# Kernel optimization log

Measured on AMD Instinct MI355X. Metric: run time of the kernel, lower is better.

The kernel has to match this reference:

```python
import jax, jax.numpy as jnp
import numpy as np

INPUT_LEN = 24
HIDDEN = 64
BATCH = 8192


def _lstm_layer(seq, Wih, Whh, bih, bhh):
    """Single torch-style LSTM layer. seq: [T, B, in] -> hs: [T, B, H].
    Gate order matches torch: i, f, g, o."""
    B = seq.shape[1]
    H = Whh.shape[1]
    b = bih + bhh
    h0 = jnp.zeros((B, H), seq.dtype)
    c0 = jnp.zeros((B, H), seq.dtype)

    def step(carry, x_t):
        h, c = carry
        gates = x_t @ Wih.T + h @ Whh.T + b  # [B, 4H]
        i, f, g, o = jnp.split(gates, 4, axis=-1)
        c = jax.nn.sigmoid(f) * c + jax.nn.sigmoid(i) * jnp.tanh(g)
        h = jax.nn.sigmoid(o) * jnp.tanh(c)
        return (h, c), h

    _, hs = jax.lax.scan(step, (h0, c0), seq)
    return hs


def setup_inputs() -> dict:
    key = jax.random.key(0)
    ks = jax.random.split(key, 16)
    H = HIDDEN
    s = 1.0 / np.sqrt(H)  # torch LSTM/Linear init scale
    u = lambda k, shape, sc: jax.random.uniform(k, shape, jnp.float32, -sc, sc)
    return {
        "x": jax.random.normal(ks[0], (BATCH, INPUT_LEN), jnp.float32),
        # LSTM layer 0 (input size 1)
        "Wih0": u(ks[1], (4 * H, 1), s),
        "Whh0": u(ks[2], (4 * H, H), s),
        "bih0": u(ks[3], (4 * H,), s),
        "bhh0": u(ks[4], (4 * H,), s),
        # LSTM layer 1 (input size H)
        "Wih1": u(ks[5], (4 * H, H), s),
        "Whh1": u(ks[6], (4 * H, H), s),
        "bih1": u(ks[7], (4 * H,), s),
        "bhh1": u(ks[8], (4 * H,), s),
        # predictor MLP: Linear(H,32) -> ReLU -> Linear(32,1)
        "W1": u(ks[9], (32, H), s),
        "b1": u(ks[10], (32,), s),
        "W2": u(ks[11], (1, 32), 1.0 / np.sqrt(32)),
        "b2": u(ks[12], (1,), 1.0 / np.sqrt(32)),
        "damping": jnp.asarray(0.1, jnp.float32),
        "steps": 20,
    }


def reference(x, Wih0, Whh0, bih0, bhh0, Wih1, Whh1, bih1, bhh1,
              W1, b1, W2, b2, damping, steps):
    cur = x[..., None]  # [B, T, 1]
    alpha = jax.nn.sigmoid(damping)
    preds = []
    prev = None
    for _ in range(steps):
        seq = jnp.transpose(cur, (1, 0, 2))  # [T, B, 1]
        h1 = _lstm_layer(seq, Wih0, Whh0, bih0, bhh0)   # [T, B, H]
        h2 = _lstm_layer(h1, Wih1, Whh1, bih1, bhh1)     # [T, B, H]
        last = h2[-1]                                     # [B, H]
        pred = jax.nn.relu(last @ W1.T + b1) @ W2.T + b2  # [B, 1]
        if prev is not None:
            # torch: pred*(1-alpha) + predictions[-1].detach()*alpha*0.5
            pred = pred * (1.0 - alpha) + jax.lax.stop_gradient(prev) * alpha * 0.5
        preds.append(pred)
        prev = pred
        cur = jnp.concatenate([cur[:, 1:, :], pred[:, None, :]], axis=1)
    return jnp.concatenate(preds, axis=1)  # [B, steps]
```

## Files before the change

kernel.cpp:

```cpp
#include <hip/hip_runtime.h>


typedef _Float16 f16x8 __attribute__((ext_vector_type(8)));
typedef float f32x4 __attribute__((ext_vector_type(4)));

#define NBLK 512
#define NTHR 256
#define SRB  160

__device__ __forceinline__ float sigm(float x) {
  float e = __builtin_amdgcn_exp2f(-1.44269504089f * x);
  return __builtin_amdgcn_rcpf(1.0f + e);
}
__device__ __forceinline__ f32x4 mfma16(uint4 a, uint4 b, f32x4 c) {
  return __builtin_amdgcn_mfma_f32_16x16x32_f16(
      __builtin_bit_cast(f16x8, a), __builtin_bit_cast(f16x8, b), c, 0, 0, 0);
}
__device__ __forceinline__ uint4 pack8s(const float* p, float s) {
  union { uint4 u; _Float16 h[8]; } r;
  #pragma unroll
  for (int i = 0; i < 8; ++i) r.h[i] = (_Float16)(p[i] * s);
  return r.u;
}

__global__ __launch_bounds__(NTHR, 2) void lstm_forecast(
    const float* __restrict__ x,
    const float* __restrict__ Wih0, const float* __restrict__ Whh0,
    const float* __restrict__ bih0, const float* __restrict__ bhh0,
    const float* __restrict__ Wih1, const float* __restrict__ Whh1,
    const float* __restrict__ bih1, const float* __restrict__ bhh1,
    const float* __restrict__ W1,   const float* __restrict__ b1,
    const float* __restrict__ W2,   const float* __restrict__ b2,
    const float* __restrict__ damping, const int* __restrict__ stepsPtr,
    float* __restrict__ out)
{
  __shared__ __align__(16) _Float16 h1s[2][16 * 80];
  __shared__ __align__(16) _Float16 h2s[2][16 * 80];
  __shared__ __align__(16) float    win[24 * 16];
  __shared__ __align__(16) float    pm[2][16];

  const int tid  = threadIdx.x;
  const int wave = tid >> 6;
  const int lane = tid & 63;
  const int cc   = lane & 15;
  const int hi   = lane >> 4;
  const int b0g  = blockIdx.x * 16;

  const float LOG2E = 1.44269504089f;

  uint4 wB0[4][2], wB1[4][2], wB2[4][2];
  float bias0v[4], wih0v[4];
  f32x4 bi1[4];
  #pragma unroll
  for (int gt = 0; gt < 4; ++gt) {
    float sc = (gt == 2) ? 2.0f * LOG2E : LOG2E;
    int row = (wave + 4 * gt) * 16 + cc;
    #pragma unroll
    for (int f = 0; f < 2; ++f) {
      int col = f * 32 + hi * 8;
      wB0[gt][f] = pack8s(Whh0 + row * 64 + col, sc);
      wB1[gt][f] = pack8s(Wih1 + row * 64 + col, sc);
      wB2[gt][f] = pack8s(Whh1 + row * 64 + col, sc);
    }
    bias0v[gt] = (bih0[row] + bhh0[row]) * sc;
    wih0v[gt]  = Wih0[row] * sc;
    float b1c  = (bih1[row] + bhh1[row]) * sc;
    #pragma unroll
    for (int r = 0; r < 4; ++r) bi1[gt][r] = b1c;
  }
  uint4 wM[2];
  {
    int row = (wave & 1) * 16 + cc;
    wM[0] = pack8s(W1 + row * 64 + hi * 8, 1.0f);
    wM[1] = pack8s(W1 + row * 64 + 32 + hi * 8, 1.0f);
  }
  const float w2v  = W2[(wave & 1) * 16 + cc];
  const float b1vv = b1[(wave & 1) * 16 + cc];
  const float alpha  = sigm(damping[0]);
  const int   nsteps = stepsPtr[0];
  const float b2v    = b2[0];

  for (int e = tid; e < 384; e += NTHR) {
    int b = e & 15, t = e >> 4;
    win[t * 16 + b] = x[(b0g + b) * 24 + t];
  }
  __syncthreads();

  float prevp = 0.0f;

  for (int s = 0; s < nsteps; ++s) {
    float c1[4] = {0, 0, 0, 0}, c2s[4] = {0, 0, 0, 0};

    {
      float4 xw = *(const float4*)&win[(s % 24) * 16 + hi * 4];
      float xr[4] = {xw.x, xw.y, xw.z, xw.w};
      #pragma unroll
      for (int r = 0; r < 4; ++r) {
        float a0 = fmaf(xr[r], wih0v[0], bias0v[0]);
        float a1 = fmaf(xr[r], wih0v[1], bias0v[1]);
        float a2 = fmaf(xr[r], wih0v[2], bias0v[2]);
        float a3 = fmaf(xr[r], wih0v[3], bias0v[3]);
        float ig = __builtin_amdgcn_rcpf(1.0f + __builtin_amdgcn_exp2f(-a0));
        float fg = __builtin_amdgcn_rcpf(1.0f + __builtin_amdgcn_exp2f(-a1));
        float gg = __builtin_amdgcn_rcpf(1.0f + __builtin_amdgcn_exp2f(-a2)) * 2.0f - 1.0f;
        float og = __builtin_amdgcn_rcpf(1.0f + __builtin_amdgcn_exp2f(-a3));
        float cv = fmaf(fg, c1[r], ig * gg);
        c1[r] = cv;
        float e2 = __builtin_amdgcn_exp2f(-2.88539008178f * cv);
        float hv = og * (__builtin_amdgcn_rcpf(1.0f + e2) * 2.0f - 1.0f);
        *(_Float16*)((char*)h1s[0] + (hi * 4 + r) * SRB + (wave * 16 + cc) * 2) =
            (_Float16)hv;
      }
    }
    __syncthreads();
    uint4 a1lo = *(uint4*)((char*)h1s[0] + cc * SRB + hi * 16);
    uint4 a1hi = *(uint4*)((char*)h1s[0] + cc * SRB + hi * 16 + 64);
    uint4 a2lo = make_uint4(0, 0, 0, 0), a2hi = make_uint4(0, 0, 0, 0);

    for (int t = 0; t < 23; ++t) {
      int pb = (t + 1) & 1;
      int ph = s + t + 1; if (ph >= 24) ph -= 24;
      float4 xw = *(const float4*)&win[ph * 16 + hi * 4];
      float xr[4] = {xw.x, xw.y, xw.z, xw.w};

      f32x4 acc1[4], acc0[4];
      #pragma unroll
      for (int gt = 0; gt < 4; ++gt) {
        f32x4 tv = mfma16(a1lo, wB1[gt][0], bi1[gt]);
        tv = mfma16(a1hi, wB1[gt][1], tv);
        tv = mfma16(a2lo, wB2[gt][0], tv);
        acc1[gt] = mfma16(a2hi, wB2[gt][1], tv);
      }
      #pragma unroll
      for (int gt = 0; gt < 4; ++gt) {
        f32x4 ai;
        #pragma unroll
        for (int r = 0; r < 4; ++r) ai[r] = fmaf(xr[r], wih0v[gt], bias0v[gt]);
        f32x4 tv = mfma16(a1lo, wB0[gt][0], ai);
        acc0[gt] = mfma16(a1hi, wB0[gt][1], tv);
      }

      #pragma unroll
      for (int r = 0; r < 4; ++r) {
        float ig = __builtin_amdgcn_rcpf(1.0f + __builtin_amdgcn_exp2f(-acc1[0][r]));
        float fg = __builtin_amdgcn_rcpf(1.0f + __builtin_amdgcn_exp2f(-acc1[1][r]));
        float gg = __builtin_amdgcn_rcpf(1.0f + __builtin_amdgcn_exp2f(-acc1[2][r])) * 2.0f - 1.0f;
        float og = __builtin_amdgcn_rcpf(1.0f + __builtin_amdgcn_exp2f(-acc1[3][r]));
        float cv = fmaf(fg, c2s[r], ig * gg);
        c2s[r] = cv;
        float e2 = __builtin_amdgcn_exp2f(-2.88539008178f * cv);
        float hv = og * (__builtin_amdgcn_rcpf(1.0f + e2) * 2.0f - 1.0f);
        *(_Float16*)((char*)h2s[pb] + (hi * 4 + r) * SRB + (wave * 16 + cc) * 2) =
            (_Float16)hv;
      }
      #pragma unroll
      for (int r = 0; r < 4; ++r) {
        float ig = __builtin_amdgcn_rcpf(1.0f + __builtin_amdgcn_exp2f(-acc0[0][r]));
        float fg = __builtin_amdgcn_rcpf(1.0f + __builtin_amdgcn_exp2f(-acc0[1][r]));
        float gg = __builtin_amdgcn_rcpf(1.0f + __builtin_amdgcn_exp2f(-acc0[2][r])) * 2.0f - 1.0f;
        float og = __builtin_amdgcn_rcpf(1.0f + __builtin_amdgcn_exp2f(-acc0[3][r]));
        float cv = fmaf(fg, c1[r], ig * gg);
        c1[r] = cv;
        float e2 = __builtin_amdgcn_exp2f(-2.88539008178f * cv);
        float hv = og * (__builtin_amdgcn_rcpf(1.0f + e2) * 2.0f - 1.0f);
        *(_Float16*)((char*)h1s[pb] + (hi * 4 + r) * SRB + (wave * 16 + cc) * 2) =
            (_Float16)hv;
      }
      __syncthreads();
      a1lo = *(uint4*)((char*)h1s[pb] + cc * SRB + hi * 16);
      a1hi = *(uint4*)((char*)h1s[pb] + cc * SRB + hi * 16 + 64);
      a2lo = *(uint4*)((char*)h2s[pb] + cc * SRB + hi * 16);
      a2hi = *(uint4*)((char*)h2s[pb] + cc * SRB + hi * 16 + 64);
    }

    {
      f32x4 acc1[4];
      #pragma unroll
      for (int gt = 0; gt < 4; ++gt) {
        f32x4 tv = mfma16(a1lo, wB1[gt][0], bi1[gt]);
        tv = mfma16(a1hi, wB1[gt][1], tv);
        tv = mfma16(a2lo, wB2[gt][0], tv);
        acc1[gt] = mfma16(a2hi, wB2[gt][1], tv);
      }
      #pragma unroll
      for (int r = 0; r < 4; ++r) {
        float ig = __builtin_amdgcn_rcpf(1.0f + __builtin_amdgcn_exp2f(-acc1[0][r]));
        float fg = __builtin_amdgcn_rcpf(1.0f + __builtin_amdgcn_exp2f(-acc1[1][r]));
        float gg = __builtin_amdgcn_rcpf(1.0f + __builtin_amdgcn_exp2f(-acc1[2][r])) * 2.0f - 1.0f;
        float og = __builtin_amdgcn_rcpf(1.0f + __builtin_amdgcn_exp2f(-acc1[3][r]));
        float cv = fmaf(fg, c2s[r], ig * gg);
        float e2 = __builtin_amdgcn_exp2f(-2.88539008178f * cv);
        float hv = og * (__builtin_amdgcn_rcpf(1.0f + e2) * 2.0f - 1.0f);
        *(_Float16*)((char*)h2s[0] + (hi * 4 + r) * SRB + (wave * 16 + cc) * 2) =
            (_Float16)hv;
      }
    }
    __syncthreads();

    if (wave < 2) {
      uint4 hflo = *(uint4*)((char*)h2s[0] + cc * SRB + hi * 16);
      uint4 hfhi = *(uint4*)((char*)h2s[0] + cc * SRB + hi * 16 + 64);
      f32x4 am;
      #pragma unroll
      for (int r = 0; r < 4; ++r) am[r] = b1vv;
      am = mfma16(hflo, wM[0], am);
      am = mfma16(hfhi, wM[1], am);
      float yp[4];
      #pragma unroll
      for (int r = 0; r < 4; ++r) yp[r] = fmaxf(am[r], 0.0f) * w2v;
      #pragma unroll
      for (int mask = 1; mask <= 8; mask <<= 1) {
        #pragma unroll
        for (int r = 0; r < 4; ++r) yp[r] += __shfl_xor(yp[r], mask);
      }
      if (cc == 0) {
        #pragma unroll
        for (int r = 0; r < 4; ++r) pm[wave][hi * 4 + r] = yp[r];
      }
    }
    __syncthreads();

    if (wave == 0 && lane < 16) {
      float y = pm[0][lane] + pm[1][lane] + b2v;
      float pd = (s == 0) ? y : fmaf(y, 1.0f - alpha, prevp * (alpha * 0.5f));
      prevp = pd;
      win[(s % 24) * 16 + lane] = pd;
      out[(long)(b0g + lane) * nsteps + s] = pd;
    }
    __syncthreads();
  }
}

extern "C" void kernel_launch(void* const* d_in, const int* in_sizes, int n_in,
                              void* d_out, int out_size, void* d_ws, size_t ws_size,
                              hipStream_t stream) {
  (void)in_sizes; (void)n_in; (void)out_size; (void)d_ws; (void)ws_size;
  lstm_forecast<<<NBLK, NTHR, 0, stream>>>(
      (const float*)d_in[0],
      (const float*)d_in[1],  (const float*)d_in[2],
      (const float*)d_in[3],  (const float*)d_in[4],
      (const float*)d_in[5],  (const float*)d_in[6],
      (const float*)d_in[7],  (const float*)d_in[8],
      (const float*)d_in[9],  (const float*)d_in[10],
      (const float*)d_in[11], (const float*)d_in[12],
      (const float*)d_in[13], (const int*)d_in[14],
      (float*)d_out);
}
```

Before: 640.2 us.

## Split LSTM gate work across two wave roles with 512-thread blocks

Doubles the threads per block and splits the gate computation between two groups of four waves. One group computes the i*g products and passes them through shared memory. The other computes the forget and output gates and updates the cell state. Each wave now holds weights for two gate tiles instead of four, which cuts register pressure and allows more waves per CU. In exchange, every timestep gets an extra barrier and a shared-memory exchange. The sigmoid/tanh products are also merged so that one reciprocal covers two gates, and the initial step skips the forget term because the cell state is zero.

```diff
diff --git a/kernel.cpp b/kernel.cpp
--- a/kernel.cpp
+++ b/kernel.cpp
@@ -5,13 +5,11 @@
 typedef float f32x4 __attribute__((ext_vector_type(4)));
 
 #define NBLK 512
-#define NTHR 256
+#define NTHR 512
 #define SRB  160
 
-__device__ __forceinline__ float sigm(float x) {
-  float e = __builtin_amdgcn_exp2f(-1.44269504089f * x);
-  return __builtin_amdgcn_rcpf(1.0f + e);
-}
+__device__ __forceinline__ float rcp_(float x) { return __builtin_amdgcn_rcpf(x); }
+__device__ __forceinline__ float exp2_(float x) { return __builtin_amdgcn_exp2f(x); }
 __device__ __forceinline__ f32x4 mfma16(uint4 a, uint4 b, f32x4 c) {
   return __builtin_amdgcn_mfma_f32_16x16x32_f16(
       __builtin_bit_cast(f16x8, a), __builtin_bit_cast(f16x8, b), c, 0, 0, 0);
@@ -23,7 +21,7 @@
   return r.u;
 }
 
-__global__ __launch_bounds__(NTHR, 2) void lstm_forecast(
+__global__ __launch_bounds__(NTHR, 4) void lstm_forecast(
     const float* __restrict__ x,
     const float* __restrict__ Wih0, const float* __restrict__ Whh0,
     const float* __restrict__ bih0, const float* __restrict__ bhh0,
@@ -36,170 +34,234 @@
 {
   __shared__ __align__(16) _Float16 h1s[2][16 * 80];
   __shared__ __align__(16) _Float16 h2s[2][16 * 80];
-  __shared__ __align__(16) float    win[24 * 16];
-  __shared__ __align__(16) float    pm[2][16];
+  __shared__ __align__(16) float igx[2][4][16][16];
+  __shared__ __align__(16) float win[24 * 16];
+  __shared__ __align__(16) float pcon[8][64];
+  __shared__ float pm[2][16];
 
   const int tid  = threadIdx.x;
   const int wave = tid >> 6;
   const int lane = tid & 63;
   const int cc   = lane & 15;
   const int hi   = lane >> 4;
+  const int role = wave >> 2;
+  const int k    = wave & 3;
   const int b0g  = blockIdx.x * 16;
-
-  const float LOG2E = 1.44269504089f;
-
-  uint4 wB0[4][2], wB1[4][2], wB2[4][2];
-  float bias0v[4], wih0v[4];
-  f32x4 bi1[4];
+  const float L2E = 1.44269504089f;
+
+  uint4 wB0[2][2], wB1[2][2], wB2[2][2];
+  float bias0u[2], wih0u[2];
+  f32x4 bi1[2];
   #pragma unroll
-  for (int gt = 0; gt < 4; ++gt) {
-    float sc = (gt == 2) ? 2.0f * LOG2E : LOG2E;
-    int row = (wave + 4 * gt) * 16 + cc;
+  for (int u = 0; u < 2; ++u) {
+    int gt = u * 2 + role;
+    float sc = (gt == 2) ? 2.0f * L2E : L2E;
+    int row = gt * 64 + k * 16 + cc;
     #pragma unroll
     for (int f = 0; f < 2; ++f) {
       int col = f * 32 + hi * 8;
-      wB0[gt][f] = pack8s(Whh0 + row * 64 + col, sc);
-      wB1[gt][f] = pack8s(Wih1 + row * 64 + col, sc);
-      wB2[gt][f] = pack8s(Whh1 + row * 64 + col, sc);
-    }
-    bias0v[gt] = (bih0[row] + bhh0[row]) * sc;
-    wih0v[gt]  = Wih0[row] * sc;
-    float b1c  = (bih1[row] + bhh1[row]) * sc;
+      wB0[u][f] = pack8s(Whh0 + row * 64 + col, sc);
+      wB1[u][f] = pack8s(Wih1 + row * 64 + col, sc);
+      wB2[u][f] = pack8s(Whh1 + row * 64 + col, sc);
+    }
+    bias0u[u] = (bih0[row] + bhh0[row]) * sc;
+    wih0u[u]  = Wih0[row] * sc;
+    float bc  = (bih1[row] + bhh1[row]) * sc;
     #pragma unroll
-    for (int r = 0; r < 4; ++r) bi1[gt][r] = b1c;
-  }
-  uint4 wM[2];
-  {
-    int row = (wave & 1) * 16 + cc;
+    for (int r = 0; r < 4; ++r) bi1[u][r] = bc;
+  }
+  uint4 wM[2] = {};
+  float w2v = 0.0f, b1vv = 0.0f;
+  if (role == 0 && k < 2) {
+    int row = k * 16 + cc;
     wM[0] = pack8s(W1 + row * 64 + hi * 8, 1.0f);
     wM[1] = pack8s(W1 + row * 64 + 32 + hi * 8, 1.0f);
-  }
-  const float w2v  = W2[(wave & 1) * 16 + cc];
-  const float b1vv = b1[(wave & 1) * 16 + cc];
-  const float alpha  = sigm(damping[0]);
+    w2v  = W2[row];
+    b1vv = b1[row];
+  }
+  const float alpha  = rcp_(1.0f + exp2_(-L2E * damping[0]));
   const int   nsteps = stepsPtr[0];
   const float b2v    = b2[0];
 
+  for (int e = tid; e < 256; e += NTHR) {
+    int gt = e >> 6, idx = e & 63;
+    float sc = (gt == 2) ? 2.0f * L2E : L2E;
+    int row = gt * 64 + idx;
+    pcon[gt][idx]     = (bih0[row] + bhh0[row]) * sc;
+    pcon[4 + gt][idx] = Wih0[row] * sc;
+  }
   for (int e = tid; e < 384; e += NTHR) {
     int b = e & 15, t = e >> 4;
     win[t * 16 + b] = x[(b0g + b) * 24 + t];
   }
   __syncthreads();
 
+  char* h1c0 = (char*)h1s[0];
+  char* h1c1 = (char*)h1s[1];
+  char* h2c0 = (char*)h2s[0];
+  char* h2c1 = (char*)h2s[1];
+
   float prevp = 0.0f;
 
   for (int s = 0; s < nsteps; ++s) {
     float c1[4] = {0, 0, 0, 0}, c2s[4] = {0, 0, 0, 0};
 
-    {
+    if (role == 1) {
+      float pb0[4], pw0[4];
+      #pragma unroll
+      for (int gt = 0; gt < 4; ++gt) {
+        pb0[gt] = pcon[gt][k * 16 + cc];
+        pw0[gt] = pcon[4 + gt][k * 16 + cc];
+      }
       float4 xw = *(const float4*)&win[(s % 24) * 16 + hi * 4];
-      float xr[4] = {xw.x, xw.y, xw.z, xw.w};
+      float xa[4] = {xw.x, xw.y, xw.z, xw.w};
       #pragma unroll
       for (int r = 0; r < 4; ++r) {
-        float a0 = fmaf(xr[r], wih0v[0], bias0v[0]);
-        float a1 = fmaf(xr[r], wih0v[1], bias0v[1]);
-        float a2 = fmaf(xr[r], wih0v[2], bias0v[2]);
-        float a3 = fmaf(xr[r], wih0v[3], bias0v[3]);
-        float ig = __builtin_amdgcn_rcpf(1.0f + __builtin_amdgcn_exp2f(-a0));
-        float fg = __builtin_amdgcn_rcpf(1.0f + __builtin_amdgcn_exp2f(-a1));
-        float gg = __builtin_amdgcn_rcpf(1.0f + __builtin_amdgcn_exp2f(-a2)) * 2.0f - 1.0f;
-        float og = __builtin_amdgcn_rcpf(1.0f + __builtin_amdgcn_exp2f(-a3));
-        float cv = fmaf(fg, c1[r], ig * gg);
-        c1[r] = cv;
-        float e2 = __builtin_amdgcn_exp2f(-2.88539008178f * cv);
-        float hv = og * (__builtin_amdgcn_rcpf(1.0f + e2) * 2.0f - 1.0f);
-        *(_Float16*)((char*)h1s[0] + (hi * 4 + r) * SRB + (wave * 16 + cc) * 2) =
-            (_Float16)hv;
+        float ai = fmaf(xa[r], pw0[0], pb0[0]);
+        float af = fmaf(xa[r], pw0[1], pb0[1]);
+        float ag = fmaf(xa[r], pw0[2], pb0[2]);
+        float ao = fmaf(xa[r], pw0[3], pb0[3]);
+        float xx = exp2_(-ai), yy = exp2_(-ag);
+        float ig = (1.0f - yy) * rcp_((1.0f + xx) * (1.0f + yy));
+        (void)af;
+        c1[r] = ig;
+        float xo = exp2_(-ao);
+        float z  = exp2_(-2.88539008178f * ig);
+        float hv = (1.0f - z) * rcp_((1.0f + xo) * (1.0f + z));
+        *(_Float16*)(h1c0 + (hi * 4 + r) * SRB + (k * 16 + cc) * 2) = (_Float16)hv;
       }
     }
     __syncthreads();
-    uint4 a1lo = *(uint4*)((char*)h1s[0] + cc * SRB + hi * 16);
-    uint4 a1hi = *(uint4*)((char*)h1s[0] + cc * SRB + hi * 16 + 64);
+    uint4 a1lo = *(uint4*)(h1c0 + cc * SRB + hi * 16);
+    uint4 a1hi = *(uint4*)(h1c0 + cc * SRB + hi * 16 + 64);
     uint4 a2lo = make_uint4(0, 0, 0, 0), a2hi = make_uint4(0, 0, 0, 0);
 
     for (int t = 0; t < 23; ++t) {
       int pb = (t + 1) & 1;
       int ph = s + t + 1; if (ph >= 24) ph -= 24;
       float4 xw = *(const float4*)&win[ph * 16 + hi * 4];
-      float xr[4] = {xw.x, xw.y, xw.z, xw.w};
-
-      f32x4 acc1[4], acc0[4];
-      #pragma unroll
-      for (int gt = 0; gt < 4; ++gt) {
-        f32x4 tv = mfma16(a1lo, wB1[gt][0], bi1[gt]);
-        tv = mfma16(a1hi, wB1[gt][1], tv);
-        tv = mfma16(a2lo, wB2[gt][0], tv);
-        acc1[gt] = mfma16(a2hi, wB2[gt][1], tv);
-      }
-      #pragma unroll
-      for (int gt = 0; gt < 4; ++gt) {
+      float xa[4] = {xw.x, xw.y, xw.z, xw.w};
+
+      f32x4 acc1[2], acc0[2];
+      #pragma unroll
+      for (int u = 0; u < 2; ++u) {
+        f32x4 tv = mfma16(a1lo, wB1[u][0], bi1[u]);
+        tv = mfma16(a1hi, wB1[u][1], tv);
+        tv = mfma16(a2lo, wB2[u][0], tv);
+        acc1[u] = mfma16(a2hi, wB2[u][1], tv);
+      }
+      #pragma unroll
+      for (int u = 0; u < 2; ++u) {
         f32x4 ai;
         #pragma unroll
-        for (int r = 0; r < 4; ++r) ai[r] = fmaf(xr[r], wih0v[gt], bias0v[gt]);
-        f32x4 tv = mfma16(a1lo, wB0[gt][0], ai);
-        acc0[gt] = mfma16(a1hi, wB0[gt][1], tv);
-      }
-
-      #pragma unroll
-      for (int r = 0; r < 4; ++r) {
-        float ig = __builtin_amdgcn_rcpf(1.0f + __builtin_amdgcn_exp2f(-acc1[0][r]));
-        float fg = __builtin_amdgcn_rcpf(1.0f + __builtin_amdgcn_exp2f(-acc1[1][r]));
-        float gg = __builtin_amdgcn_rcpf(1.0f + __builtin_amdgcn_exp2f(-acc1[2][r])) * 2.0f - 1.0f;
-        float og = __builtin_amdgcn_rcpf(1.0f + __builtin_amdgcn_exp2f(-acc1[3][r]));
-        float cv = fmaf(fg, c2s[r], ig * gg);
-        c2s[r] = cv;
-        float e2 = __builtin_amdgcn_exp2f(-2.88539008178f * cv);
-        float hv = og * (__builtin_amdgcn_rcpf(1.0f + e2) * 2.0f - 1.0f);
-        *(_Float16*)((char*)h2s[pb] + (hi * 4 + r) * SRB + (wave * 16 + cc) * 2) =
-            (_Float16)hv;
-      }
-      #pragma unroll
-      for (int r = 0; r < 4; ++r) {
-        float ig = __builtin_amdgcn_rcpf(1.0f + __builtin_amdgcn_exp2f(-acc0[0][r]));
-        float fg = __builtin_amdgcn_rcpf(1.0f + __builtin_amdgcn_exp2f(-acc0[1][r]));
-        float gg = __builtin_amdgcn_rcpf(1.0f + __builtin_amdgcn_exp2f(-acc0[2][r])) * 2.0f - 1.0f;
-        float og = __builtin_amdgcn_rcpf(1.0f + __builtin_amdgcn_exp2f(-acc0[3][r]));
-        float cv = fmaf(fg, c1[r], ig * gg);
-        c1[r] = cv;
-        float e2 = __builtin_amdgcn_exp2f(-2.88539008178f * cv);
-        float hv = og * (__builtin_amdgcn_rcpf(1.0f + e2) * 2.0f - 1.0f);
-        *(_Float16*)((char*)h1s[pb] + (hi * 4 + r) * SRB + (wave * 16 + cc) * 2) =
-            (_Float16)hv;
+        for (int r = 0; r < 4; ++r) ai[r] = fmaf(xa[r], wih0u[u], bias0u[u]);
+        f32x4 tv = mfma16(a1lo, wB0[u][0], ai);
+        acc0[u] = mfma16(a1hi, wB0[u][1], tv);
+      }
+
+      float fh1[4], po1[4], fh0[4], po0[4];
+      if (role == 0) {
+        float4 g1, g0;
+        float ig1[4], ig0[4];
+        #pragma unroll
+        for (int r = 0; r < 4; ++r) {
+          float xx = exp2_(-acc1[0][r]), yy = exp2_(-acc1[1][r]);
+          ig1[r] = (1.0f - yy) * rcp_((1.0f + xx) * (1.0f + yy));
+          float x0 = exp2_(-acc0[0][r]), y0 = exp2_(-acc0[1][r]);
+          ig0[r] = (1.0f - y0) * rcp_((1.0f + x0) * (1.0f + y0));
+        }
+        g1.x = ig1[0]; g1.y = ig1[1]; g1.z = ig1[2]; g1.w = ig1[3];
+        g0.x = ig0[0]; g0.y = ig0[1]; g0.z = ig0[2]; g0.w = ig0[3];
+        *(float4*)&igx[1][k][cc][hi * 4] = g1;
+        *(float4*)&igx[0][k][cc][hi * 4] = g0;
+      } else {
+        #pragma unroll
+        for (int r = 0; r < 4; ++r) {
+          fh1[r] = rcp_(1.0f + exp2_(-acc1[0][r]));
+          po1[r] = 1.0f + exp2_(-acc1[1][r]);
+          fh0[r] = rcp_(1.0f + exp2_(-acc0[0][r]));
+          po0[r] = 1.0f + exp2_(-acc0[1][r]);
+        }
       }
       __syncthreads();
-      a1lo = *(uint4*)((char*)h1s[pb] + cc * SRB + hi * 16);
-      a1hi = *(uint4*)((char*)h1s[pb] + cc * SRB + hi * 16 + 64);
-      a2lo = *(uint4*)((char*)h2s[pb] + cc * SRB + hi * 16);
-      a2hi = *(uint4*)((char*)h2s[pb] + cc * SRB + hi * 16 + 64);
+
+      if (role == 1) {
+        float4 g1 = *(float4*)&igx[1][k][cc][hi * 4];
+        float4 g0 = *(float4*)&igx[0][k][cc][hi * 4];
+        float gg1[4] = {g1.x, g1.y, g1.z, g1.w};
+        float gg0[4] = {g0.x, g0.y, g0.z, g0.w};
+        char* h2d = (pb ? h2c1 : h2c0);
+        char* h1d = (pb ? h1c1 : h1c0);
+        #pragma unroll
+        for (int r = 0; r < 4; ++r) {
+          c2s[r] = fmaf(fh1[r], c2s[r], gg1[r]);
+          float z = exp2_(-2.88539008178f * c2s[r]);
+          float hv = (1.0f - z) * rcp_(po1[r] * (1.0f + z));
+          *(_Float16*)(h2d + (hi * 4 + r) * SRB + (k * 16 + cc) * 2) = (_Float16)hv;
+        }
+        #pragma unroll
+        for (int r = 0; r < 4; ++r) {
+          c1[r] = fmaf(fh0[r], c1[r], gg0[r]);
+          float z = exp2_(-2.88539008178f * c1[r]);
+          float hv = (1.0f - z) * rcp_(po0[r] * (1.0f + z));
+          *(_Float16*)(h1d + (hi * 4 + r) * SRB + (k * 16 + cc) * 2) = (_Float16)hv;
+        }
+      }
+      __syncthreads();
+
+      char* h1r = (pb ? h1c1 : h1c0);
+      char* h2r = (pb ? h2c1 : h2c0);
+      a1lo = *(uint4*)(h1r + cc * SRB + hi * 16);
+      a1hi = *(uint4*)(h1r + cc * SRB + hi * 16 + 64);
+      a2lo = *(uint4*)(h2r + cc * SRB + hi * 16);
+      a2hi = *(uint4*)(h2r + cc * SRB + hi * 16 + 64);
     }
 
     {
-      f32x4 acc1[4];
-      #pragma unroll
-      for (int gt = 0; gt < 4; ++gt) {
-        f32x4 tv = mfma16(a1lo, wB1[gt][0], bi1[gt]);
-        tv = mfma16(a1hi, wB1[gt][1], tv);
-        tv = mfma16(a2lo, wB2[gt][0], tv);
-        acc1[gt] = mfma16(a2hi, wB2[gt][1], tv);
-      }
-      #pragma unroll
-      for (int r = 0; r < 4; ++r) {
-        float ig = __builtin_amdgcn_rcpf(1.0f + __builtin_amdgcn_exp2f(-acc1[0][r]));
-        float fg = __builtin_amdgcn_rcpf(1.0f + __builtin_amdgcn_exp2f(-acc1[1][r]));
-        float gg = __builtin_amdgcn_rcpf(1.0f + __builtin_amdgcn_exp2f(-acc1[2][r])) * 2.0f - 1.0f;
-        float og = __builtin_amdgcn_rcpf(1.0f + __builtin_amdgcn_exp2f(-acc1[3][r]));
-        float cv = fmaf(fg, c2s[r], ig * gg);
-        float e2 = __builtin_amdgcn_exp2f(-2.88539008178f * cv);
-        float hv = og * (__builtin_amdgcn_rcpf(1.0f + e2) * 2.0f - 1.0f);
-        *(_Float16*)((char*)h2s[0] + (hi * 4 + r) * SRB + (wave * 16 + cc) * 2) =
-            (_Float16)hv;
-      }
-    }
-    __syncthreads();
-
-    if (wave < 2) {
-      uint4 hflo = *(uint4*)((char*)h2s[0] + cc * SRB + hi * 16);
-      uint4 hfhi = *(uint4*)((char*)h2s[0] + cc * SRB + hi * 16 + 64);
+      f32x4 acc1[2];
+      #pragma unroll
+      for (int u = 0; u < 2; ++u) {
+        f32x4 tv = mfma16(a1lo, wB1[u][0], bi1[u]);
+        tv = mfma16(a1hi, wB1[u][1], tv);
+        tv = mfma16(a2lo, wB2[u][0], tv);
+        acc1[u] = mfma16(a2hi, wB2[u][1], tv);
+      }
+      float fh1[4], po1[4];
+      if (role == 0) {
+        float4 g1;
+        float ig1[4];
+        #pragma unroll
+        for (int r = 0; r < 4; ++r) {
+          float xx = exp2_(-acc1[0][r]), yy = exp2_(-acc1[1][r]);
+          ig1[r] = (1.0f - yy) * rcp_((1.0f + xx) * (1.0f + yy));
+        }
+        g1.x = ig1[0]; g1.y = ig1[1]; g1.z = ig1[2]; g1.w = ig1[3];
+        *(float4*)&igx[1][k][cc][hi * 4] = g1;
+      } else {
+        #pragma unroll
+        for (int r = 0; r < 4; ++r) {
+          fh1[r] = rcp_(1.0f + exp2_(-acc1[0][r]));
+          po1[r] = 1.0f + exp2_(-acc1[1][r]);
+        }
+      }
+      __syncthreads();
+      if (role == 1) {
+        float4 g1 = *(float4*)&igx[1][k][cc][hi * 4];
+        float gg1[4] = {g1.x, g1.y, g1.z, g1.w};
+        #pragma unroll
+        for (int r = 0; r < 4; ++r) {
+          float cv = fmaf(fh1[r], c2s[r], gg1[r]);
+          float z = exp2_(-2.88539008178f * cv);
+          float hv = (1.0f - z) * rcp_(po1[r] * (1.0f + z));
+          *(_Float16*)(h2c0 + (hi * 4 + r) * SRB + (k * 16 + cc) * 2) = (_Float16)hv;
+        }
+      }
+      __syncthreads();
+    }
+
+    if (role == 0 && k < 2) {
+      uint4 hflo = *(uint4*)(h2c0 + cc * SRB + hi * 16);
+      uint4 hfhi = *(uint4*)(h2c0 + cc * SRB + hi * 16 + 64);
       f32x4 am;
       #pragma unroll
       for (int r = 0; r < 4; ++r) am[r] = b1vv;
@@ -215,7 +277,7 @@
       }
       if (cc == 0) {
         #pragma unroll
-        for (int r = 0; r < 4; ++r) pm[wave][hi * 4 + r] = yp[r];
+        for (int r = 0; r < 4; ++r) pm[k][hi * 4 + r] = yp[r];
       }
     }
     __syncthreads();
```

Measured after the change: 848.9 us. 32.6% more time.

## Pack two independent batch groups per block with LDS atomic group barriers

Applied to the files above, without the earlier changes.

Each block now holds two independent 16-sample groups of four waves each (512 threads, 256 blocks). Every __syncthreads is replaced by a spin barrier on a per-group LDS atomic counter, so one group's waves no longer wait on the other group. The gate math is also rewritten algebraically to share reciprocals across the sigmoid and tanh terms, cutting the number of rcp instructions. The risks are spin-wait overhead, the cost of waves busy-polling LDS, and small numerical differences from the merged reciprocals.

```diff
diff --git a/kernel.cpp b/kernel.cpp
--- a/kernel.cpp
+++ b/kernel.cpp
@@ -4,14 +4,12 @@
 typedef _Float16 f16x8 __attribute__((ext_vector_type(8)));
 typedef float f32x4 __attribute__((ext_vector_type(4)));
 
-#define NBLK 512
-#define NTHR 256
+#define NBLK 256
+#define NTHR 512
 #define SRB  160
 
-__device__ __forceinline__ float sigm(float x) {
-  float e = __builtin_amdgcn_exp2f(-1.44269504089f * x);
-  return __builtin_amdgcn_rcpf(1.0f + e);
-}
+__device__ __forceinline__ float rcp_(float x) { return __builtin_amdgcn_rcpf(x); }
+__device__ __forceinline__ float exp2_(float x) { return __builtin_amdgcn_exp2f(x); }
 __device__ __forceinline__ f32x4 mfma16(uint4 a, uint4 b, f32x4 c) {
   return __builtin_amdgcn_mfma_f32_16x16x32_f16(
       __builtin_bit_cast(f16x8, a), __builtin_bit_cast(f16x8, b), c, 0, 0, 0);
@@ -21,6 +19,17 @@
   #pragma unroll
   for (int i = 0; i < 8; ++i) r.h[i] = (_Float16)(p[i] * s);
   return r.u;
+}
+__device__ __forceinline__ float gatestep(float aI, float aF, float aG, float aO,
+                                          float& cst) {
+  float xx = exp2_(-aI), xf = exp2_(-aF), yy = exp2_(-aG), xo = exp2_(-aO);
+  float P = (1.0f + xx) * (1.0f + yy);
+  float Q = 1.0f + xf;
+  float N = fmaf(cst, P * Q - P * xf, (1.0f - yy) * Q);
+  float cv = N * rcp_(P * Q);
+  cst = cv;
+  float z = exp2_(-2.88539008178f * cv);
+  return (1.0f - z) * rcp_((1.0f + xo) * (1.0f + z));
 }
 
 __global__ __launch_bounds__(NTHR, 2) void lstm_forecast(
@@ -34,27 +43,29 @@
     const float* __restrict__ damping, const int* __restrict__ stepsPtr,
     float* __restrict__ out)
 {
-  __shared__ __align__(16) _Float16 h1s[2][16 * 80];
-  __shared__ __align__(16) _Float16 h2s[2][16 * 80];
-  __shared__ __align__(16) float    win[24 * 16];
-  __shared__ __align__(16) float    pm[2][16];
+  __shared__ __align__(16) _Float16 h1s[2][2][1280];
+  __shared__ __align__(16) _Float16 h2s[2][2][1280];
+  __shared__ __align__(16) float    win[2][24 * 16];
+  __shared__ float pm[2][2][16];
+  __shared__ int   cnt[2];
 
   const int tid  = threadIdx.x;
   const int wave = tid >> 6;
   const int lane = tid & 63;
   const int cc   = lane & 15;
   const int hi   = lane >> 4;
-  const int b0g  = blockIdx.x * 16;
-
-  const float LOG2E = 1.44269504089f;
+  const int g    = wave >> 2;
+  const int wg   = wave & 3;
+  const int b0g  = blockIdx.x * 32 + g * 16;
+  const float L2E = 1.44269504089f;
 
   uint4 wB0[4][2], wB1[4][2], wB2[4][2];
   float bias0v[4], wih0v[4];
   f32x4 bi1[4];
   #pragma unroll
   for (int gt = 0; gt < 4; ++gt) {
-    float sc = (gt == 2) ? 2.0f * LOG2E : LOG2E;
-    int row = (wave + 4 * gt) * 16 + cc;
+    float sc = (gt == 2) ? 2.0f * L2E : L2E;
+    int row = (wg + 4 * gt) * 16 + cc;
     #pragma unroll
     for (int f = 0; f < 2; ++f) {
       int col = f * 32 + hi * 8;
@@ -70,58 +81,65 @@
   }
   uint4 wM[2];
   {
-    int row = (wave & 1) * 16 + cc;
+    int row = (wg & 1) * 16 + cc;
     wM[0] = pack8s(W1 + row * 64 + hi * 8, 1.0f);
     wM[1] = pack8s(W1 + row * 64 + 32 + hi * 8, 1.0f);
   }
-  const float w2v  = W2[(wave & 1) * 16 + cc];
-  const float b1vv = b1[(wave & 1) * 16 + cc];
-  const float alpha  = sigm(damping[0]);
+  const float w2v  = W2[(wg & 1) * 16 + cc];
+  const float b1vv = b1[(wg & 1) * 16 + cc];
+  const float alpha  = rcp_(1.0f + exp2_(-L2E * damping[0]));
   const int   nsteps = stepsPtr[0];
   const float b2v    = b2[0];
 
-  for (int e = tid; e < 384; e += NTHR) {
+  for (int e = (tid & 255); e < 384; e += 256) {
     int b = e & 15, t = e >> 4;
-    win[t * 16 + b] = x[(b0g + b) * 24 + t];
-  }
+    win[g][t * 16 + b] = x[(b0g + b) * 24 + t];
+  }
+  if (tid < 2) cnt[tid] = 0;
   __syncthreads();
 
+  int syncTgt = 0;
+  auto gsync = [&]() {
+    syncTgt += 4;
+    if (lane == 0)
+      __hip_atomic_fetch_add(&cnt[g], 1, __ATOMIC_RELEASE,
+                             __HIP_MEMORY_SCOPE_WORKGROUP);
+    while (__hip_atomic_load(&cnt[g], __ATOMIC_ACQUIRE,
+                             __HIP_MEMORY_SCOPE_WORKGROUP) < syncTgt) { }
+  };
+
+  char* h1b[2] = { (char*)h1s[g][0], (char*)h1s[g][1] };
+  char* h2b[2] = { (char*)h2s[g][0], (char*)h2s[g][1] };
+  float* winw = win[g];
+  const int offA = cc * SRB + hi * 16;
+  const int offS = (wg * 16 + cc) * 2;
   float prevp = 0.0f;
 
   for (int s = 0; s < nsteps; ++s) {
     float c1[4] = {0, 0, 0, 0}, c2s[4] = {0, 0, 0, 0};
 
     {
-      float4 xw = *(const float4*)&win[(s % 24) * 16 + hi * 4];
-      float xr[4] = {xw.x, xw.y, xw.z, xw.w};
-      #pragma unroll
-      for (int r = 0; r < 4; ++r) {
-        float a0 = fmaf(xr[r], wih0v[0], bias0v[0]);
-        float a1 = fmaf(xr[r], wih0v[1], bias0v[1]);
-        float a2 = fmaf(xr[r], wih0v[2], bias0v[2]);
-        float a3 = fmaf(xr[r], wih0v[3], bias0v[3]);
-        float ig = __builtin_amdgcn_rcpf(1.0f + __builtin_amdgcn_exp2f(-a0));
-        float fg = __builtin_amdgcn_rcpf(1.0f + __builtin_amdgcn_exp2f(-a1));
-        float gg = __builtin_amdgcn_rcpf(1.0f + __builtin_amdgcn_exp2f(-a2)) * 2.0f - 1.0f;
-        float og = __builtin_amdgcn_rcpf(1.0f + __builtin_amdgcn_exp2f(-a3));
-        float cv = fmaf(fg, c1[r], ig * gg);
-        c1[r] = cv;
-        float e2 = __builtin_amdgcn_exp2f(-2.88539008178f * cv);
-        float hv = og * (__builtin_amdgcn_rcpf(1.0f + e2) * 2.0f - 1.0f);
-        *(_Float16*)((char*)h1s[0] + (hi * 4 + r) * SRB + (wave * 16 + cc) * 2) =
-            (_Float16)hv;
-      }
-    }
-    __syncthreads();
-    uint4 a1lo = *(uint4*)((char*)h1s[0] + cc * SRB + hi * 16);
-    uint4 a1hi = *(uint4*)((char*)h1s[0] + cc * SRB + hi * 16 + 64);
+      float4 xw = *(const float4*)&winw[(s % 24) * 16 + hi * 4];
+      float xa[4] = {xw.x, xw.y, xw.z, xw.w};
+      #pragma unroll
+      for (int r = 0; r < 4; ++r) {
+        float hv = gatestep(fmaf(xa[r], wih0v[0], bias0v[0]),
+                            fmaf(xa[r], wih0v[1], bias0v[1]),
+                            fmaf(xa[r], wih0v[2], bias0v[2]),
+                            fmaf(xa[r], wih0v[3], bias0v[3]), c1[r]);
+        *(_Float16*)(h1b[0] + (hi * 4 + r) * SRB + offS) = (_Float16)hv;
+      }
+    }
+    gsync();
+    uint4 a1lo = *(const uint4*)(h1b[0] + offA);
+    uint4 a1hi = *(const uint4*)(h1b[0] + offA + 64);
     uint4 a2lo = make_uint4(0, 0, 0, 0), a2hi = make_uint4(0, 0, 0, 0);
 
     for (int t = 0; t < 23; ++t) {
       int pb = (t + 1) & 1;
       int ph = s + t + 1; if (ph >= 24) ph -= 24;
-      float4 xw = *(const float4*)&win[ph * 16 + hi * 4];
-      float xr[4] = {xw.x, xw.y, xw.z, xw.w};
+      float4 xw = *(const float4*)&winw[ph * 16 + hi * 4];
+      float xa[4] = {xw.x, xw.y, xw.z, xw.w};
 
       f32x4 acc1[4], acc0[4];
       #pragma unroll
@@ -135,42 +153,28 @@
       for (int gt = 0; gt < 4; ++gt) {
         f32x4 ai;
         #pragma unroll
-        for (int r = 0; r < 4; ++r) ai[r] = fmaf(xr[r], wih0v[gt], bias0v[gt]);
+        for (int r = 0; r < 4; ++r) ai[r] = fmaf(xa[r], wih0v[gt], bias0v[gt]);
         f32x4 tv = mfma16(a1lo, wB0[gt][0], ai);
         acc0[gt] = mfma16(a1hi, wB0[gt][1], tv);
       }
 
-      #pragma unroll
-      for (int r = 0; r < 4; ++r) {
-        float ig = __builtin_amdgcn_rcpf(1.0f + __builtin_amdgcn_exp2f(-acc1[0][r]));
-        float fg = __builtin_amdgcn_rcpf(1.0f + __builtin_amdgcn_exp2f(-acc1[1][r]));
-        float gg = __builtin_amdgcn_rcpf(1.0f + __builtin_amdgcn_exp2f(-acc1[2][r])) * 2.0f - 1.0f;
-        float og = __builtin_amdgcn_rcpf(1.0f + __builtin_amdgcn_exp2f(-acc1[3][r]));
-        float cv = fmaf(fg, c2s[r], ig * gg);
-        c2s[r] = cv;
-        float e2 = __builtin_amdgcn_exp2f(-2.88539008178f * cv);
-        float hv = og * (__builtin_amdgcn_rcpf(1.0f + e2) * 2.0f - 1.0f);
-        *(_Float16*)((char*)h2s[pb] + (hi * 4 + r) * SRB + (wave * 16 + cc) * 2) =
-            (_Float16)hv;
-      }
-      #pragma unroll
-      for (int r = 0; r < 4; ++r) {
-        float ig = __builtin_amdgcn_rcpf(1.0f + __builtin_amdgcn_exp2f(-acc0[0][r]));
-        float fg = __builtin_amdgcn_rcpf(1.0f + __builtin_amdgcn_exp2f(-acc0[1][r]));
-        float gg = __builtin_amdgcn_rcpf(1.0f + __builtin_amdgcn_exp2f(-acc0[2][r])) * 2.0f - 1.0f;
-        float og = __builtin_amdgcn_rcpf(1.0f + __builtin_amdgcn_exp2f(-acc0[3][r]));
-        float cv = fmaf(fg, c1[r], ig * gg);
-        c1[r] = cv;
-        float e2 = __builtin_amdgcn_exp2f(-2.88539008178f * cv);
-        float hv = og * (__builtin_amdgcn_rcpf(1.0f + e2) * 2.0f - 1.0f);
-        *(_Float16*)((char*)h1s[pb] + (hi * 4 + r) * SRB + (wave * 16 + cc) * 2) =
-            (_Float16)hv;
-      }
-      __syncthreads();
-      a1lo = *(uint4*)((char*)h1s[pb] + cc * SRB + hi * 16);
-      a1hi = *(uint4*)((char*)h1s[pb] + cc * SRB + hi * 16 + 64);
-      a2lo = *(uint4*)((char*)h2s[pb] + cc * SRB + hi * 16);
-      a2hi = *(uint4*)((char*)h2s[pb] + cc * SRB + hi * 16 + 64);
+      char* h2d = h2b[pb];
+      char* h1d = h1b[pb];
+      #pragma unroll
+      for (int r = 0; r < 4; ++r) {
+        float hv = gatestep(acc1[0][r], acc1[1][r], acc1[2][r], acc1[3][r], c2s[r]);
+        *(_Float16*)(h2d + (hi * 4 + r) * SRB + offS) = (_Float16)hv;
+      }
+      #pragma unroll
+      for (int r = 0; r < 4; ++r) {
+        float hv = gatestep(acc0[0][r], acc0[1][r], acc0[2][r], acc0[3][r], c1[r]);
+        *(_Float16*)(h1d + (hi * 4 + r) * SRB + offS) = (_Float16)hv;
+      }
+      gsync();
+      a1lo = *(const uint4*)(h1b[pb] + offA);
+      a1hi = *(const uint4*)(h1b[pb] + offA + 64);
+      a2lo = *(const uint4*)(h2b[pb] + offA);
+      a2hi = *(const uint4*)(h2b[pb] + offA + 64);
     }
 
     {
@@ -184,22 +188,16 @@
       }
       #pragma unroll
       for (int r = 0; r < 4; ++r) {
-        float ig = __builtin_amdgcn_rcpf(1.0f + __builtin_amdgcn_exp2f(-acc1[0][r]));
-        float fg = __builtin_amdgcn_rcpf(1.0f + __builtin_amdgcn_exp2f(-acc1[1][r]));
-        float gg = __builtin_amdgcn_rcpf(1.0f + __builtin_amdgcn_exp2f(-acc1[2][r])) * 2.0f - 1.0f;
-        float og = __builtin_amdgcn_rcpf(1.0f + __builtin_amdgcn_exp2f(-acc1[3][r]));
-        float cv = fmaf(fg, c2s[r], ig * gg);
-        float e2 = __builtin_amdgcn_exp2f(-2.88539008178f * cv);
-        float hv = og * (__builtin_amdgcn_rcpf(1.0f + e2) * 2.0f - 1.0f);
-        *(_Float16*)((char*)h2s[0] + (hi * 4 + r) * SRB + (wave * 16 + cc) * 2) =
-            (_Float16)hv;
-      }
-    }
-    __syncthreads();
-
-    if (wave < 2) {
-      uint4 hflo = *(uint4*)((char*)h2s[0] + cc * SRB + hi * 16);
-      uint4 hfhi = *(uint4*)((char*)h2s[0] + cc * SRB + hi * 16 + 64);
+        float cv = c2s[r];
+        float hv = gatestep(acc1[0][r], acc1[1][r], acc1[2][r], acc1[3][r], cv);
+        *(_Float16*)(h2b[0] + (hi * 4 + r) * SRB + offS) = (_Float16)hv;
+      }
+    }
+    gsync();
+
+    if (wg < 2) {
+      uint4 hflo = *(const uint4*)(h2b[0] + offA);
+      uint4 hfhi = *(const uint4*)(h2b[0] + offA + 64);
       f32x4 am;
       #pragma unroll
       for (int r = 0; r < 4; ++r) am[r] = b1vv;
@@ -215,19 +213,19 @@
       }
       if (cc == 0) {
         #pragma unroll
-        for (int r = 0; r < 4; ++r) pm[wave][hi * 4 + r] = yp[r];
-      }
-    }
-    __syncthreads();
-
-    if (wave == 0 && lane < 16) {
-      float y = pm[0][lane] + pm[1][lane] + b2v;
+        for (int r = 0; r < 4; ++r) pm[g][wg][hi * 4 + r] = yp[r];
+      }
+    }
+    gsync();
+
+    if (wg == 0 && lane < 16) {
+      float y = pm[g][0][lane] + pm[g][1][lane] + b2v;
       float pd = (s == 0) ? y : fmaf(y, 1.0f - alpha, prevp * (alpha * 0.5f));
       prevp = pd;
-      win[(s % 24) * 16 + lane] = pd;
+      winw[(s % 24) * 16 + lane] = pd;
       out[(long)(b0g + lane) * nsteps + s] = pd;
     }
-    __syncthreads();
+    gsync();
   }
 }
 
```

After: 661.6 us. +3.3%, slower.
